# Kernel optimization log

Measured on AMD Instinct MI355X. Metric: run time of the kernel, lower is better.

Reference implementation:

```python
import jax, jax.numpy as jnp
import numpy as np

N_E = 1024      # nconcepts (codebook size)
E_DIM = 64      # cdim (codebook vector dim)
BETA = 0.25
LEGACY = True


def setup_inputs() -> dict:
    key = jax.random.key(0)
    k1, k2, k3 = jax.random.split(key, 3)
    z_ = jax.random.normal(k1, (32, 256, 32, 32), jnp.float32)
    # 1x1 conv dis_modulator: 256 -> 64 channels (stored as [out, in])
    conv_w = jax.random.normal(k2, (64, 256), jnp.float32) / np.sqrt(256.0)
    conv_b = jnp.zeros((64,), jnp.float32)
    # embedding.weight.data.uniform_(-1/n_e, 1/n_e)
    emb = jax.random.uniform(k3, (N_E, E_DIM), jnp.float32, -1.0 / N_E, 1.0 / N_E)
    return {"z_": z_, "conv_w": conv_w, "conv_b": conv_b, "emb": emb}


def _forward(z_, conv_w, conv_b, emb):
    sg = jax.lax.stop_gradient
    # dis_modulator: 1x1 conv == per-pixel linear map  (B,Cin,H,W)->(B,Cout,H,W)
    z = jnp.einsum('bchw,oc->bohw', z_, conv_w) + conv_b[None, :, None, None]
    B = z.shape[0]
    # torch .view(-1, e_dim): row-major flatten of (B,C,H,W) into chunks of e_dim
    zf = z.reshape(-1, E_DIM)  # [B*C*H*W/e_dim, e_dim]

    # contrastive term: mean pairwise cosine similarity of codebook rows
    d1 = emb @ emb.T                                  # [n_e, n_e]
    norms = jnp.linalg.norm(emb, axis=1)              # [n_e]
    cosine = d1 / (norms[:, None] * norms[None, :])
    contrastive = jnp.mean(cosine)

    # squared L2 distances: ||z||^2 + ||e||^2 - 2 z.e
    d = (jnp.sum(zf * zf, axis=1, keepdims=True)
         + jnp.sum(emb * emb, axis=1)[None, :]
         - 2.0 * (zf @ emb.T))                        # [N, n_e]
    idx = jnp.argmin(d, axis=1)                       # [N]
    z_q = emb[idx].reshape(z.shape)

    if LEGACY:
        loss = jnp.mean((sg(z_q) - z) ** 2) + BETA * jnp.mean((z_q - sg(z)) ** 2)
    else:
        loss = BETA * jnp.mean((sg(z_q) - z) ** 2) + jnp.mean((z_q - sg(z)) ** 2)
    # hessian_penalty(G, z_, G_z=z): G is an affine 1x1 conv, so the central
    # second difference G(z+x) - 2G(z) + G(z-x) is identically zero -> penalty = 0.
    loss = loss + contrastive

    # straight-through estimator
    z_q_st = z + sg(z_q - z)

    # replicate source exactly: flat zeros(B*n_e) scattered at codebook indices
    sampled = jnp.zeros((B * N_E,), z.dtype).at[idx].set(1.0).reshape(B, N_E)
    min_idx = idx.reshape(B, -1)
    return z_q_st, loss, sampled, min_idx


def reference(z_, conv_w, conv_b, emb):
    z_q, loss, sampled, min_idx = _forward(z_, conv_w, conv_b, emb)
    return z_q, loss, sampled, min_idx
```

## Files before the change

kernel.cpp:

```cpp
#include <hip/hip_runtime.h>
#include <hip/hip_bf16.h>

#define NE      1024
#define ED      64
#define ZTOT    2097152
#define CIN     256
#define COUT    64
#define HW      1024

#define OFF_LOSS 2097152
#define OFF_SAMP 2097153
#define OFF_IDX  2129921

#define XSTR 68

__global__ __launch_bounds__(256) void k_prep(float* __restrict__ out_samp,
                                              const float* __restrict__ emb,
                                              float* __restrict__ enorm,
                                              float* __restrict__ cpart) {
    int bid = blockIdx.x, t = threadIdx.x;
    if (bid < 128) {
        out_samp[bid * 256 + t] = 0.0f;
        return;
    }
    int g = bid - 128;
    __shared__ float inv_s[64];
    __shared__ float S[256];
    if (t < 64) {
        int j = g * 64 + t;
        const float* e = emb + (size_t)j * ED;
        float r8[8];
        #pragma unroll
        for (int s = 0; s < 8; s++) { float v = e[s]; r8[s] = v * v; }
        #pragma unroll
        for (int m = 1; m < 8; m++) {
            #pragma unroll
            for (int s = 0; s < 8; s++) { float v = e[8 * m + s]; r8[s] += v * v; }
        }
        float en = ((r8[0] + r8[1]) + (r8[2] + r8[3])) + ((r8[4] + r8[5]) + (r8[6] + r8[7]));
        enorm[j] = en;
        inv_s[t] = 1.0f / sqrtf(en);
    }
    __syncthreads();
    int d = t & 63, q = t >> 6;
    float s = 0.0f;
    #pragma unroll
    for (int m = 0; m < 16; m++) {
        int i = q + 4 * m;
        s = fmaf(emb[(size_t)(g * 64 + i) * ED + d], inv_s[i], s);
    }
    S[t] = s;
    __syncthreads();
    if (t < 64)
        cpart[g * 64 + t] = (S[t] + S[t + 64]) + (S[t + 128] + S[t + 192]);
}

__global__ __launch_bounds__(256) void k_conv(const float* __restrict__ x,
                                              const float* __restrict__ w,
                                              const float* __restrict__ bias,
                                              float* __restrict__ z) {
    __shared__ float Xs[64 * XSTR];
    __shared__ float Ws[64 * XSTR];
    int t  = threadIdx.x;
    int b  = blockIdx.y;
    int p0 = blockIdx.x * 64;
    int pg = t & 15;
    int og = t >> 4;
    float acc[4][4];
    #pragma unroll
    for (int i = 0; i < 4; i++)
        #pragma unroll
        for (int j = 0; j < 4; j++) acc[i][j] = 0.0f;

    for (int c0 = 0; c0 < CIN; c0 += 64) {
        __syncthreads();
        {
            int u = t & 15, cg2 = t >> 4;
            #pragma unroll
            for (int m = 0; m < 4; m++) {
                int c = cg2 + 16 * m;
                float4 v = *(const float4*)&x[(size_t)(b * CIN + c0 + c) * HW + p0 + 4 * u];
                *(float4*)&Xs[c * XSTR + 4 * u] = v;
            }
            #pragma unroll
            for (int m = 0; m < 4; m++) {
                int o = cg2 + 16 * m;
                float4 v = *(const float4*)&w[o * CIN + c0 + 4 * u];
                Ws[(4 * u + 0) * XSTR + o] = v.x;
                Ws[(4 * u + 1) * XSTR + o] = v.y;
                Ws[(4 * u + 2) * XSTR + o] = v.z;
                Ws[(4 * u + 3) * XSTR + o] = v.w;
            }
        }
        __syncthreads();
        #pragma unroll 8
        for (int k = 0; k < 64; k++) {
            float4 xv = *(const float4*)&Xs[k * XSTR + 4 * pg];
            float4 wv = *(const float4*)&Ws[k * XSTR + 4 * og];
            float xa[4] = {xv.x, xv.y, xv.z, xv.w};
            float wb[4] = {wv.x, wv.y, wv.z, wv.w};
            #pragma unroll
            for (int i = 0; i < 4; i++)
                #pragma unroll
                for (int j = 0; j < 4; j++)
                    acc[i][j] = fmaf(xa[i], wb[j], acc[i][j]);
        }
    }
    #pragma unroll
    for (int j = 0; j < 4; j++) {
        int o = 4 * og + j;
        float bv = bias[o];
        float4 outv;
        outv.x = acc[0][j] + bv;
        outv.y = acc[1][j] + bv;
        outv.z = acc[2][j] + bv;
        outv.w = acc[3][j] + bv;
        *(float4*)&z[(size_t)(b * COUT + o) * HW + p0 + 4 * pg] = outv;
    }
}

__global__ __launch_bounds__(256, 2) void k_dist(const float* __restrict__ z,
                                                 const float* __restrict__ emb,
                                                 const float* __restrict__ enorm,
                                                 float* __restrict__ out_idx,
                                                 float* __restrict__ out_samp,
                                                 float* __restrict__ out_zq,
                                                 float* __restrict__ ssep) {
    __shared__ float zs[64 * 64];
    __shared__ float zn_s[64];
    __shared__ float redd[32 * 64];
    __shared__ int   redj[32 * 64];
    __shared__ int   bj_s[64];
    __shared__ float warr[4];
    int t    = threadIdx.x;
    int row0 = blockIdx.x * 64;
    int rg   = t & 7;
    int cg   = t >> 3;

    {
        int kb = t & 15, rr0 = t >> 4;
        #pragma unroll
        for (int m = 0; m < 4; m++) {
            int rr = rr0 + 16 * m;
            float4 v = *(const float4*)&z[(size_t)(row0 + rr) * 64 + 4 * kb];
            *(float4*)&zs[rr * 64 + 4 * (kb ^ (rr & 15))] = v;
        }
    }
    if (t < 64) {
        const float* zr = z + (size_t)(row0 + t) * 64;
        float r8[8];
        #pragma unroll
        for (int s = 0; s < 8; s++) { float v = zr[s]; r8[s] = v * v; }
        #pragma unroll
        for (int m = 1; m < 8; m++) {
            #pragma unroll
            for (int s = 0; s < 8; s++) { float v = zr[8 * m + s]; r8[s] += v * v; }
        }
        zn_s[t] = ((r8[0] + r8[1]) + (r8[2] + r8[3])) + ((r8[4] + r8[5]) + (r8[6] + r8[7]));
    }
    __syncthreads();

    float znr[8];
    #pragma unroll
    for (int i = 0; i < 8; i++) znr[i] = zn_s[rg + 8 * i];

    float bestd[8];
    int   bestj[8];
    #pragma unroll
    for (int i = 0; i < 8; i++) { bestd[i] = __builtin_huge_valf(); bestj[i] = 0; }

    for (int pass = 0; pass < 4; pass++) {
        float acc[8][8];
        #pragma unroll
        for (int i = 0; i < 8; i++)
            #pragma unroll
            for (int j = 0; j < 8; j++) acc[i][j] = 0.0f;

        const float* ebase = emb + ((size_t)(pass * 256 + cg) << 6);
        for (int kb = 0; kb < 16; kb++) {
            float4 za[8];
            #pragma unroll
            for (int i = 0; i < 8; i++) {
                int rr = rg + 8 * i;
                za[i] = *(const float4*)&zs[rr * 64 + 4 * (kb ^ (rr & 15))];
            }
            #pragma unroll
            for (int j = 0; j < 8; j++) {
                float4 ev = *(const float4*)&ebase[((size_t)(32 * j) << 6) + 4 * kb];
                #pragma unroll
                for (int i = 0; i < 8; i++) {
                    acc[i][j] = fmaf(za[i].x, ev.x, acc[i][j]);
                    acc[i][j] = fmaf(za[i].y, ev.y, acc[i][j]);
                    acc[i][j] = fmaf(za[i].z, ev.z, acc[i][j]);
                    acc[i][j] = fmaf(za[i].w, ev.w, acc[i][j]);
                }
            }
        }
        #pragma unroll
        for (int j = 0; j < 8; j++) {
            int c = pass * 256 + cg + 32 * j;
            float en = enorm[c];
            #pragma unroll
            for (int i = 0; i < 8; i++) {
                float A = znr[i] + en;
                float D = A - 2.0f * acc[i][j];
                if (D < bestd[i]) { bestd[i] = D; bestj[i] = c; }
            }
        }
    }

    #pragma unroll
    for (int i = 0; i < 8; i++) {
        redd[cg * 64 + rg + 8 * i] = bestd[i];
        redj[cg * 64 + rg + 8 * i] = bestj[i];
    }
    __syncthreads();
    if (t < 64) {
        float bd = __builtin_huge_valf();
        int   bj = 0x7fffffff;
        #pragma unroll
        for (int c = 0; c < 32; c++) {
            float dd = redd[c * 64 + t];
            int   jj = redj[c * 64 + t];
            if (dd < bd || (dd == bd && jj < bj)) { bd = dd; bj = jj; }
        }
        bj_s[t] = bj;
        out_idx[row0 + t] = (float)bj;
        atomicExch(&out_samp[bj], 1.0f);
    }
    __syncthreads();

    {
        int r  = t & 63;
        int kq = t >> 6;
        int bj = bj_s[r];
        const float* er = emb + ((size_t)bj << 6) + kq * 16;
        float sq = 0.0f;
        #pragma unroll
        for (int m = 0; m < 4; m++) {
            int kb = 4 * kq + m;
            float4 zv = *(const float4*)&zs[r * 64 + 4 * (kb ^ (r & 15))];
            float4 ev = *(const float4*)&er[4 * m];
            float d0 = ev.x - zv.x, d1 = ev.y - zv.y, d2 = ev.z - zv.z, d3 = ev.w - zv.w;
            float4 o4;
            o4.x = zv.x + d0; o4.y = zv.y + d1; o4.z = zv.z + d2; o4.w = zv.w + d3;
            *(float4*)&out_zq[((size_t)(row0 + r) << 6) + 4 * kb] = o4;
            sq += d0 * d0; sq += d1 * d1; sq += d2 * d2; sq += d3 * d3;
        }
        #pragma unroll
        for (int off = 32; off > 0; off >>= 1) sq += __shfl_down(sq, off, 64);
        if ((t & 63) == 0) warr[t >> 6] = sq;
    }
    __syncthreads();
    if (t == 0)
        ssep[blockIdx.x] = (warr[0] + warr[1]) + (warr[2] + warr[3]);
}

__global__ __launch_bounds__(256) void k_final(const float* __restrict__ ssep,
                                               const float* __restrict__ cpart,
                                               float* __restrict__ out_loss) {
    __shared__ double SD[256];
    __shared__ float  CS;
    int t = threadIdx.x;
    SD[t] = (double)ssep[t] + (double)ssep[t + 256];
    __syncthreads();
    #pragma unroll
    for (int off = 128; off > 0; off >>= 1) {
        if (t < off) SD[t] += SD[t + off];
        __syncthreads();
    }
    if (t < 64) {
        float v = 0.0f;
        #pragma unroll
        for (int m = 0; m < 16; m++) v += cpart[m * 64 + t];
        float sq = v * v;
        #pragma unroll
        for (int off = 32; off > 0; off >>= 1) sq += __shfl_down(sq, off, 64);
        if (t == 0) CS = sq / (1024.0f * 1024.0f);
    }
    __syncthreads();
    if (t == 0) {
        float m = (float)(SD[0] / (double)ZTOT);
        out_loss[0] = (m + 0.25f * m) + CS;
    }
}

extern "C" void kernel_launch(void* const* d_in, const int* in_sizes, int n_in,
                              void* d_out, int out_size, void* d_ws, size_t ws_size,
                              hipStream_t stream) {
    (void)in_sizes; (void)n_in; (void)out_size; (void)ws_size;
    const float* z_     = (const float*)d_in[0];
    const float* conv_w = (const float*)d_in[1];
    const float* conv_b = (const float*)d_in[2];
    const float* emb    = (const float*)d_in[3];

    float* out      = (float*)d_out;
    float* out_zq   = out;
    float* out_loss = out + OFF_LOSS;
    float* out_samp = out + OFF_SAMP;
    float* out_idx  = out + OFF_IDX;

    char*   ws    = (char*)d_ws;
    float*  wz    = (float*)ws;
    float*  enorm = (float*)(ws + 8388608);
    float*  cpart = enorm + 1024;
    float*  ssep  = cpart + 1024;

    k_prep <<<144, 256, 0, stream>>>(out_samp, emb, enorm, cpart);
    k_conv <<<dim3(16, 32), 256, 0, stream>>>(z_, conv_w, conv_b, wz);
    k_dist <<<512, 256, 0, stream>>>(wz, emb, enorm, out_idx, out_samp, out_zq, ssep);
    k_final<<<1, 256, 0, stream>>>(ssep, cpart, out_loss);
}
```

Before: 181.5 us.

## Stage transposed codebook in LDS and tile distance GEMM with 128-row blocks

Adds a transposed copy of the codebook built in the prep kernel and changes the distance kernel to process 128 rows per block. Each block loops over 8 chunks of 128 codewords staged into shared memory, and both z and codebook tiles are held k-major so each inner step is an 8x8 outer product from shared memory instead of reading the codebook from global memory per thread. The argmin reduction now uses wave shuffles followed by a small cross-wave merge. In exchange the grid is halved to 256 blocks, shared memory per block grows, and a barrier is added for each chunk load.

```diff
diff --git a/kernel.cpp b/kernel.cpp
--- a/kernel.cpp
+++ b/kernel.cpp
@@ -13,46 +13,78 @@
 #define OFF_IDX  2129921
 
 #define XSTR 68
+#define TSTR 132
 
 __global__ __launch_bounds__(256) void k_prep(float* __restrict__ out_samp,
                                               const float* __restrict__ emb,
                                               float* __restrict__ enorm,
-                                              float* __restrict__ cpart) {
+                                              float* __restrict__ cpart,
+                                              float* __restrict__ embT) {
     int bid = blockIdx.x, t = threadIdx.x;
     if (bid < 128) {
         out_samp[bid * 256 + t] = 0.0f;
         return;
     }
-    int g = bid - 128;
-    __shared__ float inv_s[64];
-    __shared__ float S[256];
-    if (t < 64) {
-        int j = g * 64 + t;
-        const float* e = emb + (size_t)j * ED;
-        float r8[8];
-        #pragma unroll
-        for (int s = 0; s < 8; s++) { float v = e[s]; r8[s] = v * v; }
-        #pragma unroll
-        for (int m = 1; m < 8; m++) {
-            #pragma unroll
-            for (int s = 0; s < 8; s++) { float v = e[8 * m + s]; r8[s] += v * v; }
-        }
-        float en = ((r8[0] + r8[1]) + (r8[2] + r8[3])) + ((r8[4] + r8[5]) + (r8[6] + r8[7]));
-        enorm[j] = en;
-        inv_s[t] = 1.0f / sqrtf(en);
-    }
-    __syncthreads();
-    int d = t & 63, q = t >> 6;
-    float s = 0.0f;
-    #pragma unroll
-    for (int m = 0; m < 16; m++) {
-        int i = q + 4 * m;
-        s = fmaf(emb[(size_t)(g * 64 + i) * ED + d], inv_s[i], s);
-    }
-    S[t] = s;
-    __syncthreads();
-    if (t < 64)
-        cpart[g * 64 + t] = (S[t] + S[t + 64]) + (S[t + 128] + S[t + 192]);
+    if (bid < 144) {
+        int g = bid - 128;
+        __shared__ float inv_s[64];
+        __shared__ float S[256];
+        if (t < 64) {
+            int j = g * 64 + t;
+            const float* e = emb + (size_t)j * ED;
+            float r8[8];
+            #pragma unroll
+            for (int s = 0; s < 8; s++) { float v = e[s]; r8[s] = v * v; }
+            #pragma unroll
+            for (int m = 1; m < 8; m++) {
+                #pragma unroll
+                for (int s = 0; s < 8; s++) { float v = e[8 * m + s]; r8[s] += v * v; }
+            }
+            float en = ((r8[0] + r8[1]) + (r8[2] + r8[3])) + ((r8[4] + r8[5]) + (r8[6] + r8[7]));
+            enorm[j] = en;
+            inv_s[t] = 1.0f / sqrtf(en);
+        }
+        __syncthreads();
+        int d = t & 63, q = t >> 6;
+        float s = 0.0f;
+        #pragma unroll
+        for (int m = 0; m < 16; m++) {
+            int i = q + 4 * m;
+            s = fmaf(emb[(size_t)(g * 64 + i) * ED + d], inv_s[i], s);
+        }
+        S[t] = s;
+        __syncthreads();
+        if (t < 64)
+            cpart[g * 64 + t] = (S[t] + S[t + 64]) + (S[t + 128] + S[t + 192]);
+        return;
+    }
+    int g2 = bid - 144;
+    int c0 = g2 * 64;
+    __shared__ float tl[64 * 68];
+    {
+        int cc = t >> 2, q = t & 3;
+        const float* src = emb + ((size_t)(c0 + cc) << 6) + 16 * q;
+        #pragma unroll
+        for (int m = 0; m < 4; m++) {
+            float4 v = *(const float4*)&src[4 * m];
+            *(float4*)&tl[cc * 68 + 16 * q + 4 * m] = v;
+        }
+    }
+    __syncthreads();
+    {
+        int k = t >> 2, uq = t & 3;
+        float* dst = embT + ((size_t)k << 10) + c0 + 16 * uq;
+        #pragma unroll
+        for (int m = 0; m < 4; m++) {
+            int cc = 16 * uq + 4 * m;
+            float4 v;
+            v.x = tl[(cc + 0) * 68 + k];
+            v.y = tl[(cc + 1) * 68 + k];
+            v.z = tl[(cc + 2) * 68 + k];
+            v.w = tl[(cc + 3) * 68 + k];
+            *(float4*)&dst[4 * m] = v;
+        }
+    }
 }
 
 __global__ __launch_bounds__(256) void k_conv(const float* __restrict__ x,
@@ -120,34 +152,40 @@
 }
 
 __global__ __launch_bounds__(256, 2) void k_dist(const float* __restrict__ z,
+                                                 const float* __restrict__ embT,
                                                  const float* __restrict__ emb,
                                                  const float* __restrict__ enorm,
                                                  float* __restrict__ out_idx,
                                                  float* __restrict__ out_samp,
                                                  float* __restrict__ out_zq,
                                                  float* __restrict__ ssep) {
-    __shared__ float zs[64 * 64];
-    __shared__ float zn_s[64];
-    __shared__ float redd[32 * 64];
-    __shared__ int   redj[32 * 64];
-    __shared__ int   bj_s[64];
+    __shared__ float zs[64 * TSTR];
+    __shared__ float es[64 * TSTR];
+    __shared__ float zn_s[128];
+    __shared__ float bwd[4 * 128];
+    __shared__ int   bwj[4 * 128];
+    __shared__ int   bj_s[128];
     __shared__ float warr[4];
     int t    = threadIdx.x;
-    int row0 = blockIdx.x * 64;
-    int rg   = t & 7;
-    int cg   = t >> 3;
+    int row0 = blockIdx.x * 128;
+    int rg   = t & 15;
+    int cg   = t >> 4;
 
     {
-        int kb = t & 15, rr0 = t >> 4;
-        #pragma unroll
-        for (int m = 0; m < 4; m++) {
-            int rr = rr0 + 16 * m;
-            float4 v = *(const float4*)&z[(size_t)(row0 + rr) * 64 + 4 * kb];
-            *(float4*)&zs[rr * 64 + 4 * (kb ^ (rr & 15))] = v;
-        }
-    }
-    if (t < 64) {
-        const float* zr = z + (size_t)(row0 + t) * 64;
+        int r = t >> 1, kh = (t & 1) * 32;
+        const float* zr = z + ((size_t)(row0 + r) << 6) + kh;
+        #pragma unroll
+        for (int m = 0; m < 8; m++) {
+            float4 v = *(const float4*)&zr[4 * m];
+            int k = kh + 4 * m;
+            zs[(k + 0) * TSTR + r] = v.x;
+            zs[(k + 1) * TSTR + r] = v.y;
+            zs[(k + 2) * TSTR + r] = v.z;
+            zs[(k + 3) * TSTR + r] = v.w;
+        }
+    }
+    if (t < 128) {
+        const float* zr = z + ((size_t)(row0 + t) << 6);
         float r8[8];
         #pragma unroll
         for (int s = 0; s < 8; s++) { float v = zr[s]; r8[s] = v * v; }
@@ -162,43 +200,50 @@
 
     float znr[8];
     #pragma unroll
-    for (int i = 0; i < 8; i++) znr[i] = zn_s[rg + 8 * i];
+    for (int i = 0; i < 8; i++)
+        znr[i] = zn_s[4 * rg + (i & 3) + 64 * (i >> 2)];
 
     float bestd[8];
     int   bestj[8];
     #pragma unroll
-    for (int i = 0; i < 8; i++) { bestd[i] = __builtin_huge_valf(); bestj[i] = 0; }
-
-    for (int pass = 0; pass < 4; pass++) {
+    for (int i = 0; i < 8; i++) { bestd[i] = __builtin_huge_valf(); bestj[i] = 0x7fffffff; }
+
+    for (int ch = 0; ch < 8; ch++) {
+        __syncthreads();
+        {
+            int k = t >> 2, uq = t & 3;
+            const float* src = embT + ((size_t)k << 10) + ch * 128 + 32 * uq;
+            float* dst = es + k * TSTR + 32 * uq;
+            #pragma unroll
+            for (int m = 0; m < 8; m++)
+                *(float4*)&dst[4 * m] = *(const float4*)&src[4 * m];
+        }
+        __syncthreads();
+
         float acc[8][8];
         #pragma unroll
         for (int i = 0; i < 8; i++)
             #pragma unroll
             for (int j = 0; j < 8; j++) acc[i][j] = 0.0f;
 
-        const float* ebase = emb + ((size_t)(pass * 256 + cg) << 6);
-        for (int kb = 0; kb < 16; kb++) {
-            float4 za[8];
-            #pragma unroll
-            for (int i = 0; i < 8; i++) {
-                int rr = rg + 8 * i;
-                za[i] = *(const float4*)&zs[rr * 64 + 4 * (kb ^ (rr & 15))];
-            }
-            #pragma unroll
-            for (int j = 0; j < 8; j++) {
-                float4 ev = *(const float4*)&ebase[((size_t)(32 * j) << 6) + 4 * kb];
+        #pragma unroll 4
+        for (int k = 0; k < 64; k++) {
+            float4 za1 = *(const float4*)&zs[k * TSTR + 4 * rg];
+            float4 za2 = *(const float4*)&zs[k * TSTR + 64 + 4 * rg];
+            float4 ev1 = *(const float4*)&es[k * TSTR + 4 * cg];
+            float4 ev2 = *(const float4*)&es[k * TSTR + 64 + 4 * cg];
+            float zr8[8] = {za1.x, za1.y, za1.z, za1.w, za2.x, za2.y, za2.z, za2.w};
+            float er8[8] = {ev1.x, ev1.y, ev1.z, ev1.w, ev2.x, ev2.y, ev2.z, ev2.w};
+            #pragma unroll
+            for (int i = 0; i < 8; i++)
                 #pragma unroll
-                for (int i = 0; i < 8; i++) {
-                    acc[i][j] = fmaf(za[i].x, ev.x, acc[i][j]);
-                    acc[i][j] = fmaf(za[i].y, ev.y, acc[i][j]);
-                    acc[i][j] = fmaf(za[i].z, ev.z, acc[i][j]);
-                    acc[i][j] = fmaf(za[i].w, ev.w, acc[i][j]);
-                }
-            }
-        }
+                for (int j = 0; j < 8; j++)
+                    acc[i][j] = fmaf(zr8[i], er8[j], acc[i][j]);
+        }
+
         #pragma unroll
         for (int j = 0; j < 8; j++) {
-            int c = pass * 256 + cg + 32 * j;
+            int c = ch * 128 + 4 * cg + (j & 3) + 64 * (j >> 2);
             float en = enorm[c];
             #pragma unroll
             for (int i = 0; i < 8; i++) {
@@ -211,17 +256,24 @@
 
     #pragma unroll
     for (int i = 0; i < 8; i++) {
-        redd[cg * 64 + rg + 8 * i] = bestd[i];
-        redj[cg * 64 + rg + 8 * i] = bestj[i];
-    }
-    __syncthreads();
-    if (t < 64) {
-        float bd = __builtin_huge_valf();
-        int   bj = 0x7fffffff;
-        #pragma unroll
-        for (int c = 0; c < 32; c++) {
-            float dd = redd[c * 64 + t];
-            int   jj = redj[c * 64 + t];
+        float d = bestd[i]; int j = bestj[i];
+        float d2 = __shfl_down(d, 32, 64); int j2 = __shfl_down(j, 32, 64);
+        if (d2 < d || (d2 == d && j2 < j)) { d = d2; j = j2; }
+        d2 = __shfl_down(d, 16, 64); j2 = __shfl_down(j, 16, 64);
+        if (d2 < d || (d2 == d && j2 < j)) { d = d2; j = j2; }
+        if ((t & 63) < 16) {
+            int rl = 4 * (t & 15) + (i & 3) + 64 * (i >> 2);
+            bwd[(t >> 6) * 128 + rl] = d;
+            bwj[(t >> 6) * 128 + rl] = j;
+        }
+    }
+    __syncthreads();
+    if (t < 128) {
+        float bd = bwd[t]; int bj = bwj[t];
+        #pragma unroll
+        for (int w2 = 1; w2 < 4; w2++) {
+            float dd = bwd[w2 * 128 + t];
+            int   jj = bwj[w2 * 128 + t];
             if (dd < bd || (dd == bd && jj < bj)) { bd = dd; bj = jj; }
         }
         bj_s[t] = bj;
@@ -231,20 +283,23 @@
     __syncthreads();
 
     {
-        int r  = t & 63;
-        int kq = t >> 6;
-        int bj = bj_s[r];
-        const float* er = emb + ((size_t)bj << 6) + kq * 16;
+        int rl = t & 127, kh = (t >> 7) * 32;
+        int bj = bj_s[rl];
+        const float* er = emb + ((size_t)bj << 6) + kh;
+        float* oz = out_zq + ((size_t)(row0 + rl) << 6) + kh;
         float sq = 0.0f;
         #pragma unroll
-        for (int m = 0; m < 4; m++) {
-            int kb = 4 * kq + m;
-            float4 zv = *(const float4*)&zs[r * 64 + 4 * (kb ^ (r & 15))];
+        for (int m = 0; m < 8; m++) {
             float4 ev = *(const float4*)&er[4 * m];
-            float d0 = ev.x - zv.x, d1 = ev.y - zv.y, d2 = ev.z - zv.z, d3 = ev.w - zv.w;
+            int k = kh + 4 * m;
+            float z0 = zs[(k + 0) * TSTR + rl];
+            float z1 = zs[(k + 1) * TSTR + rl];
+            float z2 = zs[(k + 2) * TSTR + rl];
+            float z3 = zs[(k + 3) * TSTR + rl];
+            float d0 = ev.x - z0, d1 = ev.y - z1, d2 = ev.z - z2, d3 = ev.w - z3;
             float4 o4;
-            o4.x = zv.x + d0; o4.y = zv.y + d1; o4.z = zv.z + d2; o4.w = zv.w + d3;
-            *(float4*)&out_zq[((size_t)(row0 + r) << 6) + 4 * kb] = o4;
+            o4.x = z0 + d0; o4.y = z1 + d1; o4.z = z2 + d2; o4.w = z3 + d3;
+            *(float4*)&oz[4 * m] = o4;
             sq += d0 * d0; sq += d1 * d1; sq += d2 * d2; sq += d3 * d3;
         }
         #pragma unroll
@@ -262,7 +317,7 @@
     __shared__ double SD[256];
     __shared__ float  CS;
     int t = threadIdx.x;
-    SD[t] = (double)ssep[t] + (double)ssep[t + 256];
+    SD[t] = (double)ssep[t];
     __syncthreads();
     #pragma unroll
     for (int off = 128; off > 0; off >>= 1) {
@@ -300,14 +355,16 @@
     float* out_samp = out + OFF_SAMP;
     float* out_idx  = out + OFF_IDX;
 
-    char*   ws    = (char*)d_ws;
-    float*  wz    = (float*)ws;
-    float*  enorm = (float*)(ws + 8388608);
-    float*  cpart = enorm + 1024;
-    float*  ssep  = cpart + 1024;
-
-    k_prep <<<144, 256, 0, stream>>>(out_samp, emb, enorm, cpart);
+    float* ws    = (float*)d_ws;
+    float* wz    = ws;
+    float* embT  = ws + 2097152;
+    float* enorm = ws + 2162688;
+    float* cpart = ws + 2163712;
+    float* ssep  = ws + 2164736;
+
+    k_prep <<<160, 256, 0, stream>>>(out_samp, emb, enorm, cpart, embT);
     k_conv <<<dim3(16, 32), 256, 0, stream>>>(z_, conv_w, conv_b, wz);
-    k_dist <<<512, 256, 0, stream>>>(wz, emb, enorm, out_idx, out_samp, out_zq, ssep);
+    k_dist <<<256, 256, 0, stream>>>(wz, embT, emb, enorm, out_idx, out_samp,
+                                     out_zq, ssep);
     k_final<<<1, 256, 0, stream>>>(ssep, cpart, out_loss);
 }
```

New measurement: 177.0 us. 2.5% less time.
